# Kernel optimization log

Measured on AMD Instinct MI355X. Metric: run time of the kernel, lower is better.

## Reference

```python
import jax, jax.numpy as jnp
import numpy as np

B, S, D, L = 16, 2048, 256, 4  # batch, seq, embedding_dim, num_blocks
NUM_FEATS = 6  # time features; +1 price = 7 input channels


def _layernorm(x, g, b):
    mu = x.mean(-1, keepdims=True)
    var = x.var(-1, keepdims=True)
    return (x - mu) * jax.lax.rsqrt(var + 1e-5) * g + b


def _slstm(gx, Wh):
    """sLSTM with exponential gating + max stabilizer.
    gx: [S, B, 4D] input-side pre-activations; Wh: [D, 4D] recurrent weights.
    Returns hidden states [S, B, D]."""
    d = Wh.shape[0]
    b = gx.shape[1]
    z0 = jnp.zeros((b, d), gx.dtype)
    init = (z0, z0, z0, z0)  # c, n, h, m

    def step(carry, gx_t):
        c, n, h, m = carry
        g = gx_t + h @ Wh
        i_t, f_t, z_t, o_t = jnp.split(g, 4, axis=-1)
        m_new = jnp.maximum(f_t + m, i_t)          # stabilizer state
        i_p = jnp.exp(i_t - m_new)                 # exp input gate
        f_p = jnp.exp(f_t + m - m_new)             # exp forget gate
        c = f_p * c + i_p * jnp.tanh(z_t)
        n = f_p * n + i_p                          # normalizer
        h = jax.nn.sigmoid(o_t) * c / jnp.maximum(jnp.abs(n), 1.0)
        return (c, n, h, m_new), h

    _, hs = jax.lax.scan(step, init, gx)
    return hs


def setup_inputs() -> dict:
    key = jax.random.key(0)
    ks = jax.random.split(key, 10)
    s = 0.02
    return {
        "x": jax.random.normal(ks[0], (B, S), jnp.float32),
        "time_features": jax.random.normal(ks[1], (B, S, NUM_FEATS), jnp.float32),
        "in_W": jax.random.normal(ks[2], (NUM_FEATS + 1, D), jnp.float32) * s,
        "in_b": jnp.zeros((D,), jnp.float32),
        "ln_g": jnp.ones((L, D), jnp.float32),
        "ln_b": jnp.zeros((L, D), jnp.float32),
        "Wx": jax.random.normal(ks[3], (L, D, 4 * D), jnp.float32) * s,
        "Wh": jax.random.normal(ks[4], (L, D, 4 * D), jnp.float32) * s,
        "bg": jnp.zeros((L, 4 * D), jnp.float32),
        "fc_W": jax.random.normal(ks[5], (D, 1), jnp.float32) * s,
        "fc_b": jnp.zeros((1,), jnp.float32),
    }


def reference(x, time_features, in_W, in_b, ln_g, ln_b, Wx, Wh, bg, fc_W, fc_b):
    # concat price + time features -> [B, S, 7]; project to embedding_dim
    feats = jnp.concatenate([x[..., None], time_features], axis=-1)
    h = feats @ in_W + in_b  # [B, S, D]
    nblocks = ln_g.shape[0]
    for l in range(nblocks):  # fixed small layer count
        xn = _layernorm(h, ln_g[l], ln_b[l])
        gx = jnp.einsum("bsd,de->bse", xn, Wx[l]) + bg[l]  # [B,S,4D]
        hs = _slstm(gx.transpose(1, 0, 2), Wh[l])          # [S,B,D]
        h = h + hs.transpose(1, 0, 2)                       # residual
    # dropout is identity in eval mode
    return h[:, -1, :] @ fc_W + fc_b  # [B, 1]
```

## Files before the change

kernel.cpp:

```cpp
#include <hip/hip_runtime.h>

#define BB 16
#define SS 2048
#define DD 256
#define ND4 1024
#define PRD 16
#define PGD 8
#define HLP 4

typedef __attribute__((ext_vector_type(8))) _Float16 half8;
typedef __attribute__((ext_vector_type(4))) float f32x4;
typedef __attribute__((ext_vector_type(4))) unsigned int u32x4;
typedef unsigned long long u64;
union H8 { half8 v; unsigned int u[4]; uint4 q; };
union U4 { u32x4 v; unsigned int u[4]; };

__device__ __forceinline__ u64 aload(const u64* p) {
    return __hip_atomic_load(p, __ATOMIC_RELAXED, __HIP_MEMORY_SCOPE_AGENT);
}
__device__ __forceinline__ void astore(u64* p, u64 v) {
    __hip_atomic_store(p, v, __ATOMIC_RELAXED, __HIP_MEMORY_SCOPE_AGENT);
}
__device__ __forceinline__ void wgstore(u64* p, u64 v) {
    __hip_atomic_store(p, v, __ATOMIC_RELAXED, __HIP_MEMORY_SCOPE_WORKGROUP);
}
__device__ __forceinline__ unsigned pload(const unsigned* p) {
    return __hip_atomic_load(p, __ATOMIC_RELAXED, __HIP_MEMORY_SCOPE_AGENT);
}
__device__ __forceinline__ void pstore(unsigned* p, unsigned v) {
    __hip_atomic_store(p, v, __ATOMIC_RELAXED, __HIP_MEMORY_SCOPE_AGENT);
}
__device__ __forceinline__ int aflag(int* p) {
    return __hip_atomic_load(p, __ATOMIC_RELAXED, __HIP_MEMORY_SCOPE_AGENT);
}
__device__ __forceinline__ void sflag(int* p) {
    __hip_atomic_store(p, 1, __ATOMIC_RELAXED, __HIP_MEMORY_SCOPE_AGENT);
}
__device__ __forceinline__ unsigned short f16b(float x) {
    union { _Float16 h; unsigned short u; } c; c.h = (_Float16)x; return c.u;
}
__device__ __forceinline__ unsigned umin2(unsigned a, unsigned b) { return a < b ? a : b; }
__device__ __forceinline__ bool spinBail(int& guard, int* af) {
    if ((++guard & 63) == 0) {
        __builtin_amdgcn_s_sleep(1);
        if (guard > (1 << 18) || aflag(af)) { sflag(af); return true; }
    }
    return false;
}

__global__ void embed_kernel(const float* __restrict__ x, const float* __restrict__ tf,
                             const float* __restrict__ inW, const float* __restrict__ inb,
                             float* __restrict__ h) {
    int tok = blockIdx.x, d = threadIdx.x;
    float xv = x[tok];
    float acc = inb[d] + xv * inW[d];
#pragma unroll
    for (int c = 0; c < 6; ++c)
        acc = fmaf(tf[tok * 6 + c], inW[(c + 1) * DD + d], acc);
    h[(size_t)tok * DD + d] = acc;
}

__global__ void wxprep_kernel(const float* __restrict__ Wx, unsigned short* __restrict__ Wxh) {
    int l = blockIdx.x >> 6, G = blockIdx.x & 63;
    int lane = threadIdx.x, quad = lane >> 4, mm = lane & 15;
    const float* W = Wx + (size_t)l * DD * ND4;
    unsigned short* o = Wxh + (size_t)blockIdx.x * 4096;
#pragma unroll
    for (int kc = 0; kc < 8; ++kc) {
        __align__(16) unsigned short tmp[8];
#pragma unroll
        for (int i = 0; i < 8; ++i)
            tmp[i] = f16b(W[(size_t)(kc * 32 + quad * 8 + i) * ND4 + G * 16 + mm]);
        *(uint4*)(o + ((size_t)kc * 64 + lane) * 8) = *(uint4*)tmp;
    }
}

__global__ __launch_bounds__(256, 1) void mega_kernel(
    const float* __restrict__ hemb, const float* __restrict__ Wh,
    const float* __restrict__ lng, const float* __restrict__ lnb,
    const float* __restrict__ bgp, const unsigned short* __restrict__ Wxh,
    float* __restrict__ hout,
    u64* __restrict__ Xbuf, u64* __restrict__ Rbuf, u64* __restrict__ GXbuf,
    unsigned* __restrict__ prog, int* __restrict__ abortFlag) {
    __shared__ __align__(16) char smemBlob[57344];
    __shared__ int fastFlag;
    const int bid = blockIdx.x;
    const int tid = threadIdx.x;
    const int xslot = bid & 7;
    const int ksl = bid >> 3;
    const int l = xslot >> 1;
    const bool isScan = ((xslot & 1) == 0);
    if (!isScan && ksl >= HLP) return;

    if (isScan) {
        const int g = ksl;
        const int w = tid >> 6, lane = tid & 63;
        const int mm = lane & 15, quad = lane >> 4;
        const int sb = tid >> 4, sd = tid & 15;
        const int dglob = g * 16 + sd;
        float (*gbuf)[4][16][16] = (float (*)[4][16][16])smemBlob;

        unsigned* xt = prog + 32 + l * 16;
        if (tid == 0) {
            unsigned xcc;
            asm volatile("s_getreg_b32 %0, hwreg(HW_REG_XCC_ID)" : "=s"(xcc));
            pstore(xt + g, xcc + 1u);
        }

        H8 bfr[8];
        {
            const float* WhL = Wh + (size_t)l * DD * ND4;
            const int col = w * 256 + g * 16 + mm;
#pragma unroll
            for (int kc = 0; kc < 8; ++kc)
#pragma unroll
                for (int p = 0; p < 4; ++p) {
                    float f0 = WhL[(size_t)(32 * kc + 8 * quad + 2 * p) * ND4 + col];
                    float f1 = WhL[(size_t)(32 * kc + 8 * quad + 2 * p + 1) * ND4 + col];
                    bfr[kc].u[p] = (unsigned)f16b(f0) | ((unsigned)f16b(f1) << 16);
                }
        }

        if (tid == 0) {
            bool plOK = true;
            {
                unsigned ref = 0;
                for (int i = 0; i < 16; ++i) {
                    unsigned v = 0; int gu = 0;
                    for (;;) { v = pload(xt + i); if (v) break; if (++gu > (1 << 18)) break; }
                    if (v == 0) { plOK = false; break; }
                    if (i == 0) ref = v; else plOK &= (v == ref);
                }
            }
            unsigned* ready  = prog + 96 + l * 16;
            unsigned* result = prog + 160 + l * 16;
            u64* tw = (u64*)(prog + 24) + l;
            const u64 MAGIC = 0x5A5A5A5ADEADBEEFULL;
            if (!plOK) {
                pstore(result + g, 1u);
            } else if (g == 0) {
                int gu = 0; bool all;
                do {
                    all = true;
                    for (int i = 1; i < 16; ++i) all &= (pload(ready + i) != 0);
                } while (!all && ++gu < (1 << 20));
                wgstore(tw, MAGIC);
                pstore(result + 0, 2u);
            } else {
                u64 acc = 0;
                for (int i = 0; i < 64; ++i) acc |= *(volatile const u64*)tw;
                pstore(ready + g, 1u);
                int ok = (acc == MAGIC) ? 1 : 0, post = 0, gu = 0;
                while (!ok) {
                    u64 v;
                    asm volatile("buffer_inv sc0\n\t"
                                 "global_load_dwordx2 %0, %1, off\n\t"
                                 "s_waitcnt vmcnt(0)"
                                 : "=v"(v) : "v"(tw) : "memory");
                    if (v == MAGIC) { ok = 1; break; }
                    if (pload(result + 0) == 2u && ++post > 512) break;
                    if (++gu > (1 << 20)) break;
                }
                pstore(result + g, ok ? 2u : 1u);
            }
            bool allok = true; int gu2 = 0;
            for (int i = 0; i < 16; ++i) {
                unsigned v;
                for (;;) {
                    v = pload(result + i);
                    if (v) break;
                    if ((++gu2 & 1023) == 0) __builtin_amdgcn_s_sleep(1);
                    if (gu2 > (1 << 22)) break;
                }
                allok &= (v == 2u);
            }
            fastFlag = allok ? 1 : 0;
        }

        float c_ = 0.f, n_ = 0.f, m_ = 0.f;

        u64* Xl = Xbuf + (size_t)l * 4096;
        const u64* Rprev = Rbuf + (size_t)(l > 0 ? l - 1 : 0) * PRD * 4096;
        u64* Rcur = Rbuf + (size_t)(l < 3 ? l : 0) * PRD * 4096;
        const u64* GXl = GXbuf + (size_t)l * PGD * 16384;

        const int pquad = (dglob >> 3) & 3;
        const int ppair = (sd >> 1) & 3;
        const size_t pubIdx = (size_t)(g >> 1) * 256 + (size_t)pquad * 64 + (size_t)sb * 4 + ppair;
        const bool doPub = (sd & 1) == 0;
        const size_t rdBase = (size_t)quad * 64 + (size_t)mm * 4;
        const size_t gxIdx = (size_t)sb * 1024 + dglob;
        const size_t rIdx = (size_t)sb * 256 + dglob;
        const float* hemb0 = hemb + (size_t)sb * SS * DD + dglob;
        float* hrow = hout + (size_t)sb * SS * DD + dglob;

        unsigned psC = 0, minPgC = 0;
        const unsigned* psP = prog + (l + 1);
        const unsigned* pgP = prog + 4 + (l + 1) * 4;

        u64 pf0, pf1, pf2, pf3, pfr = 0;
        float pfh = 0.f;
        {
            const u64* Gp = GXl + gxIdx;
            pf0 = aload(Gp); pf1 = aload(Gp + 256);
            pf2 = aload(Gp + 512); pf3 = aload(Gp + 768);
            if (l > 0) pfr = aload(Rprev + rIdx);
            else pfh = hemb0[0];
        }
        __syncthreads();
        const bool fastX = (fastFlag != 0);

        auto issuePF = [&](int t1) {
            const u64* Gp1 = GXl + (size_t)(t1 & (PGD - 1)) * 16384 + gxIdx;
            pf0 = aload(Gp1); pf1 = aload(Gp1 + 256);
            pf2 = aload(Gp1 + 512); pf3 = aload(Gp1 + 768);
            if (l > 0) pfr = aload(Rprev + (size_t)(t1 & (PRD - 1)) * 4096 + rIdx);
            else pfh = hemb0[(size_t)t1 * DD];
        };

        for (int t = 0; t < SS; ++t) {
            const unsigned tagT = (unsigned)(t + 1);
            float gxi, gxf, gxz, gxoo, hin;
            {
                u64 a0 = pf0, a1 = pf1, a2 = pf2, a3 = pf3, ar = pfr;
                bool ok = ((unsigned)(a0 >> 32) == tagT) & ((unsigned)(a1 >> 32) == tagT) &
                          ((unsigned)(a2 >> 32) == tagT) & ((unsigned)(a3 >> 32) == tagT) &
                          ((l == 0) | ((unsigned)(ar >> 32) == tagT));
                if (!ok) {
                    const u64* Gp = GXl + (size_t)(t & (PGD - 1)) * 16384 + gxIdx;
                    const u64* Rp = Rprev + (size_t)(t & (PRD - 1)) * 4096 + rIdx;
                    int guard = 0;
                    for (;;) {
                        a0 = aload(Gp); a1 = aload(Gp + 256);
                        a2 = aload(Gp + 512); a3 = aload(Gp + 768);
                        if (l > 0) ar = aload(Rp);
                        ok = ((unsigned)(a0 >> 32) == tagT) & ((unsigned)(a1 >> 32) == tagT) &
                             ((unsigned)(a2 >> 32) == tagT) & ((unsigned)(a3 >> 32) == tagT) &
                             ((l == 0) | ((unsigned)(ar >> 32) == tagT));
                        if (ok) break;
                        if (spinBail(guard, abortFlag)) break;
                    }
                }
                gxi = __uint_as_float((unsigned)a0);
                gxf = __uint_as_float((unsigned)a1);
                gxz = __uint_as_float((unsigned)a2);
                gxoo = __uint_as_float((unsigned)a3);
                hin = (l > 0) ? __uint_as_float((unsigned)ar) : pfh;
            }
            f32x4 acc0 = {0.f, 0.f, 0.f, 0.f}, acc1 = {0.f, 0.f, 0.f, 0.f};
            if (t > 0) {
                const unsigned tag = (unsigned)t;
                const u64* Xp = Xl + (size_t)(t & 1) * 2048 + rdBase;
                H8 afr[8];
                if (fastX) {
                    U4 q[16];
                    const u64* b0 = Xp;
                    const u64* b1 = Xp + 512;
                    const u64* b2 = Xp + 1024;
                    const u64* b3 = Xp + 1536;
                    int guard = 0;
                    for (;;) {
                        asm volatile(
                            "buffer_inv sc0\n\t"
                            "global_load_dwordx4 %0,  %16, off\n\t"
                            "global_load_dwordx4 %1,  %16, off offset:16\n\t"
                            "global_load_dwordx4 %2,  %16, off offset:2048\n\t"
                            "global_load_dwordx4 %3,  %16, off offset:2064\n\t"
                            "global_load_dwordx4 %4,  %17, off\n\t"
                            "global_load_dwordx4 %5,  %17, off offset:16\n\t"
                            "global_load_dwordx4 %6,  %17, off offset:2048\n\t"
                            "global_load_dwordx4 %7,  %17, off offset:2064\n\t"
                            "global_load_dwordx4 %8,  %18, off\n\t"
                            "global_load_dwordx4 %9,  %18, off offset:16\n\t"
                            "global_load_dwordx4 %10, %18, off offset:2048\n\t"
                            "global_load_dwordx4 %11, %18, off offset:2064\n\t"
                            "global_load_dwordx4 %12, %19, off\n\t"
                            "global_load_dwordx4 %13, %19, off offset:16\n\t"
                            "global_load_dwordx4 %14, %19, off offset:2048\n\t"
                            "global_load_dwordx4 %15, %19, off offset:2064\n\t"
                            "s_waitcnt vmcnt(0)"
                            : "=&v"(q[0].v), "=&v"(q[1].v), "=&v"(q[2].v), "=&v"(q[3].v),
                              "=&v"(q[4].v), "=&v"(q[5].v), "=&v"(q[6].v), "=&v"(q[7].v),
                              "=&v"(q[8].v), "=&v"(q[9].v), "=&v"(q[10].v), "=&v"(q[11].v),
                              "=&v"(q[12].v), "=&v"(q[13].v), "=&v"(q[14].v), "=&v"(q[15].v)
                            : "v"(b0), "v"(b1), "v"(b2), "v"(b3)
                            : "memory");
                        bool ok = true;
#pragma unroll
                        for (int i = 0; i < 16; ++i)
                            ok &= (q[i].u[1] == tag) & (q[i].u[3] == tag);
                        if (ok) break;
                        if ((++guard & 255) == 0) {
                            if (guard > (1 << 18) || aflag(abortFlag)) { sflag(abortFlag); break; }
                        }
                    }
#pragma unroll
                    for (int kc = 0; kc < 8; ++kc) {
                        afr[kc].u[0] = q[kc * 2].u[0];
                        afr[kc].u[1] = q[kc * 2].u[2];
                        afr[kc].u[2] = q[kc * 2 + 1].u[0];
                        afr[kc].u[3] = q[kc * 2 + 1].u[2];
                    }
                } else {
                    u64 v[32];
                    int guard = 0;
                    for (;;) {
#pragma unroll
                        for (int kc = 0; kc < 8; ++kc)
#pragma unroll
                            for (int p = 0; p < 4; ++p)
                                v[kc * 4 + p] = aload(Xp + (size_t)kc * 256 + p);
                        bool ok = true;
#pragma unroll
                        for (int i = 0; i < 32; ++i) ok &= ((unsigned)(v[i] >> 32) == tag);
                        if (ok) break;
                        if ((++guard & 255) == 0) {
                            if (guard > (1 << 18) || aflag(abortFlag)) { sflag(abortFlag); break; }
                        }
                    }
#pragma unroll
                    for (int kc = 0; kc < 8; ++kc)
#pragma unroll
                        for (int p = 0; p < 4; ++p) afr[kc].u[p] = (unsigned)v[kc * 4 + p];
                }
                issuePF(t + 1 < SS ? t + 1 : t);
                acc0 = __builtin_amdgcn_mfma_f32_16x16x32_f16(afr[0].v, bfr[0].v, acc0, 0, 0, 0);
                acc1 = __builtin_amdgcn_mfma_f32_16x16x32_f16(afr[1].v, bfr[1].v, acc1, 0, 0, 0);
                acc0 = __builtin_amdgcn_mfma_f32_16x16x32_f16(afr[2].v, bfr[2].v, acc0, 0, 0, 0);
                acc1 = __builtin_amdgcn_mfma_f32_16x16x32_f16(afr[3].v, bfr[3].v, acc1, 0, 0, 0);
                acc0 = __builtin_amdgcn_mfma_f32_16x16x32_f16(afr[4].v, bfr[4].v, acc0, 0, 0, 0);
                acc1 = __builtin_amdgcn_mfma_f32_16x16x32_f16(afr[5].v, bfr[5].v, acc1, 0, 0, 0);
                acc0 = __builtin_amdgcn_mfma_f32_16x16x32_f16(afr[6].v, bfr[6].v, acc0, 0, 0, 0);
                acc1 = __builtin_amdgcn_mfma_f32_16x16x32_f16(afr[7].v, bfr[7].v, acc1, 0, 0, 0);
            } else {
                issuePF(1);
            }
            if (g == 0 && tid == 0) pstore(prog + l, (unsigned)(t + 1));
            f32x4 acc = acc0 + acc1;
            const int par = t & 1;
#pragma unroll
            for (int r = 0; r < 4; ++r) gbuf[par][w][quad * 4 + r][mm] = acc[r];
            __syncthreads();
            float gi = gbuf[par][0][sb][sd] + gxi;
            float gf = gbuf[par][1][sb][sd] + gxf;
            float gz = gbuf[par][2][sb][sd] + gxz;
            float go = gbuf[par][3][sb][sd] + gxoo;
            float mn = fmaxf(gf + m_, gi);
            float ip = __expf(gi - mn);
            float fp = __expf(gf + m_ - mn);
            float e2z = __expf(2.f * gz);
            float th = 1.f - 2.f * __builtin_amdgcn_rcpf(e2z + 1.f);
            c_ = fp * c_ + ip * th;
            n_ = fp * n_ + ip;
            m_ = mn;
            float sg = __builtin_amdgcn_rcpf(1.f + __expf(-go));
            float hval = sg * c_ * __builtin_amdgcn_rcpf(fmaxf(fabsf(n_), 1.f));
            float rnew = hin + hval;
            float hodd = __shfl_down(hval, 1);
            if (doPub) {
                unsigned payload = (unsigned)f16b(hval) | ((unsigned)f16b(hodd) << 16);
                u64 pv = ((u64)tagT << 32) | (u64)payload;
                u64* dst = Xl + (size_t)((t + 1) & 1) * 2048 + pubIdx;
                if (fastX) wgstore(dst, pv);
                else astore(dst, pv);
            }
            if (l == 3) {
                hrow[(size_t)t * DD] = rnew;
            } else {
                if (t >= PRD) {
                    unsigned needT = (unsigned)(t - PRD);
                    if (!((psC >= needT + 2) & (minPgC >= needT + 1))) {
                        int guard = 0;
                        for (;;) {
                            unsigned a  = pload(psP);
                            unsigned b0 = pload(pgP + 0);
                            unsigned b1 = pload(pgP + 1);
                            unsigned b2 = pload(pgP + 2);
                            unsigned b3 = pload(pgP + 3);
                            unsigned mn4 = umin2(umin2(b0, b1), umin2(b2, b3));
                            psC = a; minPgC = mn4;
                            if ((a >= needT + 2) & (mn4 >= needT + 1)) break;
                            if (spinBail(guard, abortFlag)) break;
                        }
                    }
                }
                astore(Rcur + (size_t)(t & (PRD - 1)) * 4096 + rIdx,
                       ((u64)tagT << 32) | (u64)__float_as_uint(rnew));
            }
            __syncthreads();
        }
    } else {
        const int j = ksl;
        const int w = tid >> 6, lane = tid & 63;
        const int mm = lane & 15, quad = lane >> 4;
        const int hb_ = tid >> 4, hd0 = (tid & 15) * 16;
        unsigned short (*hA)[264] = (unsigned short (*)[264])smemBlob;

        const u64* Rin = Rbuf + (size_t)(l > 0 ? l - 1 : 0) * PRD * 4096;
        u64* GXl = GXbuf + (size_t)l * PGD * 16384;
        const unsigned short* WxL = Wxh + (size_t)l * 262144;
        const float* lngL = lng + l * DD;
        const float* lnbL = lnb + l * DD;
        const float* bgL = bgp + (size_t)l * ND4;
        unsigned* myProg = prog + 4 + l * 4 + j;
        const unsigned* scanProg = prog + l;
        unsigned spC = 0;

        for (int t = j; t < SS; t += HLP) {
            const unsigned tagT = (unsigned)(t + 1);
            float rv[16];
            if (l == 0) {
                const float4* p = (const float4*)(hemb + ((size_t)hb_ * SS + t) * DD + hd0);
#pragma unroll
                for (int q4 = 0; q4 < 4; ++q4) {
                    float4 f = p[q4];
                    rv[q4 * 4 + 0] = f.x; rv[q4 * 4 + 1] = f.y;
                    rv[q4 * 4 + 2] = f.z; rv[q4 * 4 + 3] = f.w;
                }
            } else {
                const u64* Rp = Rin + (size_t)(t & (PRD - 1)) * 4096 + (size_t)tid * 16;
                int guard = 0;
                for (;;) {
                    u64 vv[16];
#pragma unroll
                    for (int i = 0; i < 16; ++i) vv[i] = aload(Rp + i);
                    bool ok = true;
#pragma unroll
                    for (int i = 0; i < 16; ++i) ok &= ((unsigned)(vv[i] >> 32) == tagT);
                    if (ok) {
#pragma unroll
                        for (int i = 0; i < 16; ++i) rv[i] = __uint_as_float((unsigned)vv[i]);
                        break;
                    }
                    if (spinBail(guard, abortFlag)) {
#pragma unroll
                        for (int i = 0; i < 16; ++i) rv[i] = 0.f;
                        break;
                    }
                }
            }
            float s = 0.f, ssq = 0.f;
#pragma unroll
            for (int i = 0; i < 16; ++i) { s += rv[i]; ssq += rv[i] * rv[i]; }
#pragma unroll
            for (int msk = 1; msk < 16; msk <<= 1) {
                s += __shfl_xor(s, msk);
                ssq += __shfl_xor(ssq, msk);
            }
            float muv = s * (1.f / 256.f);
            float rsv = rsqrtf(fmaxf(ssq * (1.f / 256.f) - muv * muv, 0.f) + 1e-5f);
            {
                __align__(16) unsigned short ov[16];
#pragma unroll
                for (int i = 0; i < 16; ++i)
                    ov[i] = f16b((rv[i] - muv) * rsv * lngL[hd0 + i] + lnbL[hd0 + i]);
                *(uint4*)&hA[hb_][hd0] = *(uint4*)&ov[0];
                *(uint4*)&hA[hb_][hd0 + 8] = *(uint4*)&ov[8];
            }
            __syncthreads();
            if (tid == 0) pstore(myProg, (unsigned)(t + 1));
            H8 A[8];
#pragma unroll
            for (int kc = 0; kc < 8; ++kc)
                A[kc].q = *(const uint4*)&hA[mm][kc * 32 + quad * 8];
            f32x4 acc[16];
            const unsigned short* WxW = WxL + (size_t)w * 16 * 4096;
#pragma unroll
            for (int n = 0; n < 16; ++n) {
                const unsigned short* bp = WxW + (size_t)n * 4096 + (size_t)lane * 8;
                f32x4 a = {0.f, 0.f, 0.f, 0.f};
#pragma unroll
                for (int kc = 0; kc < 8; ++kc) {
                    H8 B;
                    B.q = *(const uint4*)(bp + (size_t)kc * 512);
                    a = __builtin_amdgcn_mfma_f32_16x16x32_f16(A[kc].v, B.v, a, 0, 0, 0);
                }
                acc[n] = a;
            }
            if (t >= PGD) {
                unsigned need = (unsigned)(t - PGD) + 2;
                if (spC < need) {
                    int guard = 0;
                    for (;;) {
                        unsigned v = pload(scanProg);
                        spC = v;
                        if (v >= need) break;
                        if (spinBail(guard, abortFlag)) break;
                    }
                }
            }
            u64* Gq = GXl + (size_t)(t & (PGD - 1)) * 16384;
#pragma unroll
            for (int n = 0; n < 16; ++n) {
                int c = (w * 16 + n) * 16 + mm;
                float bgv = bgL[c];
                f32x4 a = acc[n];
#pragma unroll
                for (int r = 0; r < 4; ++r)
                    astore(Gq + (size_t)(quad * 4 + r) * 1024 + c,
                           ((u64)tagT << 32) | (u64)__float_as_uint(a[r] + bgv));
            }
            __syncthreads();
        }
    }
}

__global__ void final_kernel(const float* __restrict__ h, const float* __restrict__ fcW,
                             const float* __restrict__ fcb, float* __restrict__ out) {
    int b = blockIdx.x, lane = threadIdx.x;
    const float4 hv = *(const float4*)(h + ((size_t)b * SS + (SS - 1)) * DD + lane * 4);
    const float4 wv = *(const float4*)(fcW + lane * 4);
    float s = hv.x * wv.x + hv.y * wv.y + hv.z * wv.z + hv.w * wv.w;
#pragma unroll
    for (int off = 32; off; off >>= 1) s += __shfl_down(s, off);
    if (lane == 0) out[b] = s + fcb[0];
}

extern "C" void kernel_launch(void* const* d_in, const int* in_sizes, int n_in,
                              void* d_out, int out_size, void* d_ws, size_t ws_size,
                              hipStream_t stream) {
    const float* x   = (const float*)d_in[0];
    const float* tf  = (const float*)d_in[1];
    const float* inW = (const float*)d_in[2];
    const float* inb = (const float*)d_in[3];
    const float* lng = (const float*)d_in[4];
    const float* lnb = (const float*)d_in[5];
    const float* Wx  = (const float*)d_in[6];
    const float* Wh  = (const float*)d_in[7];
    const float* bg  = (const float*)d_in[8];
    const float* fcW = (const float*)d_in[9];
    const float* fcb = (const float*)d_in[10];
    float* out = (float*)d_out;

    const size_t nTok = (size_t)BB * SS;
    float* hemb = (float*)d_ws;
    float* hout = hemb + nTok * DD;
    unsigned short* Wxh = (unsigned short*)(hout + nTok * DD);
    u64* Xbuf = (u64*)(Wxh + 1048576);
    u64* Rbuf = Xbuf + 4 * 2 * 2048;
    u64* GXbuf = Rbuf + 3 * PRD * 4096;
    unsigned* prog = (unsigned*)(GXbuf + 4 * PGD * 16384);
    int* abortFlag = (int*)(prog + 20);

    const size_t needed = (size_t)((char*)(prog + 256) - (char*)d_ws);
    if (ws_size < needed) return;

    hipMemsetAsync(prog, 0, 256 * sizeof(unsigned), stream);

    embed_kernel<<<nTok, DD, 0, stream>>>(x, tf, inW, inb, hemb);
    wxprep_kernel<<<4 * 64, 64, 0, stream>>>(Wx, Wxh);
    mega_kernel<<<128, 256, 0, stream>>>(hemb, Wh, lng, lnb, bg, Wxh, hout,
                                         Xbuf, Rbuf, GXbuf, prog, abortFlag);
    final_kernel<<<BB, 64, 0, stream>>>(hout, fcW, fcb, out);
    (void)in_sizes; (void)n_in; (void)out_size;
}
```

Baseline: 6.804 ms.

## Replace per-element tag polling with per-block arrival counters for recurrent exchange

```diff
diff --git a/kernel.cpp b/kernel.cpp
--- a/kernel.cpp
+++ b/kernel.cpp
@@ -29,6 +29,9 @@
 }
 __device__ __forceinline__ void pstore(unsigned* p, unsigned v) {
     __hip_atomic_store(p, v, __ATOMIC_RELAXED, __HIP_MEMORY_SCOPE_AGENT);
+}
+__device__ __forceinline__ void pwgstore(unsigned* p, unsigned v) {
+    __hip_atomic_store(p, v, __ATOMIC_RELAXED, __HIP_MEMORY_SCOPE_WORKGROUP);
 }
 __device__ __forceinline__ int aflag(int* p) {
     return __hip_atomic_load(p, __ATOMIC_RELAXED, __HIP_MEMORY_SCOPE_AGENT);
@@ -134,8 +137,10 @@
             }
             unsigned* ready  = prog + 96 + l * 16;
             unsigned* result = prog + 160 + l * 16;
-            u64* tw = (u64*)(prog + 24) + l;
-            const u64 MAGIC = 0x5A5A5A5ADEADBEEFULL;
+            u64* tw = (u64*)(prog + 384 + l * 16);
+            u64* pw = (u64*)(prog + 448 + l * 16);
+            const u64 MAGIC  = 0x5A5A5A5ADEADBEEFULL;
+            const u64 MAGIC2 = 0x1234ABCD9876EF01ULL;
             if (!plOK) {
                 pstore(result + g, 1u);
             } else if (g == 0) {
@@ -144,20 +149,32 @@
                     all = true;
                     for (int i = 1; i < 16; ++i) all &= (pload(ready + i) != 0);
                 } while (!all && ++gu < (1 << 20));
+                wgstore(pw, MAGIC2);
+                asm volatile("s_waitcnt vmcnt(0)" ::: "memory");
                 wgstore(tw, MAGIC);
                 pstore(result + 0, 2u);
             } else {
-                u64 acc = 0;
+                u64 acc = 0, accp = 0;
                 for (int i = 0; i < 64; ++i) acc |= *(volatile const u64*)tw;
+                accp = *(volatile const u64*)pw;
                 pstore(ready + g, 1u);
-                int ok = (acc == MAGIC) ? 1 : 0, post = 0, gu = 0;
+                int ok = (acc == MAGIC && accp == MAGIC2) ? 1 : 0;
+                int post = 0, gu = 0;
                 while (!ok) {
                     u64 v;
                     asm volatile("buffer_inv sc0\n\t"
                                  "global_load_dwordx2 %0, %1, off\n\t"
                                  "s_waitcnt vmcnt(0)"
                                  : "=v"(v) : "v"(tw) : "memory");
-                    if (v == MAGIC) { ok = 1; break; }
+                    if (v == MAGIC) {
+                        u64 v2;
+                        asm volatile("buffer_inv sc0\n\t"
+                                     "global_load_dwordx2 %0, %1, off\n\t"
+                                     "s_waitcnt vmcnt(0)"
+                                     : "=v"(v2) : "v"(pw) : "memory");
+                        ok = (v2 == MAGIC2) ? 1 : 0;
+                        break;
+                    }
                     if (pload(result + 0) == 2u && ++post > 512) break;
                     if (++gu > (1 << 20)) break;
                 }
@@ -193,6 +210,9 @@
         const size_t rIdx = (size_t)sb * 256 + dglob;
         const float* hemb0 = hemb + (size_t)sb * SS * DD + dglob;
         float* hrow = hout + (size_t)sb * SS * DD + dglob;
+
+        const unsigned* arrL = prog + 256 + l * 16;
+        unsigned* arrW = prog + 256 + l * 16 + g;
 
         unsigned psC = 0, minPgC = 0;
         const unsigned* psP = prog + (l + 1);
@@ -253,55 +273,93 @@
                 const u64* Xp = Xl + (size_t)(t & 1) * 2048 + rdBase;
                 H8 afr[8];
                 if (fastX) {
-                    U4 q[16];
-                    const u64* b0 = Xp;
-                    const u64* b1 = Xp + 512;
-                    const u64* b2 = Xp + 1024;
-                    const u64* b3 = Xp + 1536;
-                    int guard = 0;
-                    for (;;) {
-                        asm volatile(
-                            "buffer_inv sc0\n\t"
-                            "global_load_dwordx4 %0,  %16, off\n\t"
-                            "global_load_dwordx4 %1,  %16, off offset:16\n\t"
-                            "global_load_dwordx4 %2,  %16, off offset:2048\n\t"
-                            "global_load_dwordx4 %3,  %16, off offset:2064\n\t"
-                            "global_load_dwordx4 %4,  %17, off\n\t"
-                            "global_load_dwordx4 %5,  %17, off offset:16\n\t"
-                            "global_load_dwordx4 %6,  %17, off offset:2048\n\t"
-                            "global_load_dwordx4 %7,  %17, off offset:2064\n\t"
-                            "global_load_dwordx4 %8,  %18, off\n\t"
-                            "global_load_dwordx4 %9,  %18, off offset:16\n\t"
-                            "global_load_dwordx4 %10, %18, off offset:2048\n\t"
-                            "global_load_dwordx4 %11, %18, off offset:2064\n\t"
-                            "global_load_dwordx4 %12, %19, off\n\t"
-                            "global_load_dwordx4 %13, %19, off offset:16\n\t"
-                            "global_load_dwordx4 %14, %19, off offset:2048\n\t"
-                            "global_load_dwordx4 %15, %19, off offset:2064\n\t"
-                            "s_waitcnt vmcnt(0)"
-                            : "=&v"(q[0].v), "=&v"(q[1].v), "=&v"(q[2].v), "=&v"(q[3].v),
-                              "=&v"(q[4].v), "=&v"(q[5].v), "=&v"(q[6].v), "=&v"(q[7].v),
-                              "=&v"(q[8].v), "=&v"(q[9].v), "=&v"(q[10].v), "=&v"(q[11].v),
-                              "=&v"(q[12].v), "=&v"(q[13].v), "=&v"(q[14].v), "=&v"(q[15].v)
-                            : "v"(b0), "v"(b1), "v"(b2), "v"(b3)
-                            : "memory");
-                        bool ok = true;
-#pragma unroll
-                        for (int i = 0; i < 16; ++i)
-                            ok &= (q[i].u[1] == tag) & (q[i].u[3] == tag);
-                        if (ok) break;
-                        if ((++guard & 255) == 0) {
-                            if (guard > (1 << 18) || aflag(abortFlag)) { sflag(abortFlag); break; }
+                    {
+                        const unsigned needA = (unsigned)t;
+                        int guard = 0;
+                        for (;;) {
+                            unsigned av;
+                            asm volatile("buffer_inv sc0\n\t"
+                                         "global_load_dword %0, %1, off\n\t"
+                                         "s_waitcnt vmcnt(0)"
+                                         : "=v"(av)
+                                         : "v"(arrL + (lane & 15)) : "memory");
+                            if (__all((int)(av >= needA))) break;
+                            if ((++guard & 255) == 0) {
+                                if (guard > (1 << 18) || aflag(abortFlag)) { sflag(abortFlag); break; }
+                            }
                         }
                     }
+                    bool okp = true;
 #pragma unroll
                     for (int kc = 0; kc < 8; ++kc) {
-                        afr[kc].u[0] = q[kc * 2].u[0];
-                        afr[kc].u[1] = q[kc * 2].u[2];
-                        afr[kc].u[2] = q[kc * 2 + 1].u[0];
-                        afr[kc].u[3] = q[kc * 2 + 1].u[2];
+                        const uint4* p2 = (const uint4*)(Xp + (size_t)kc * 256);
+                        uint4 qa = p2[0], qb = p2[1];
+                        afr[kc].u[0] = qa.x; afr[kc].u[1] = qa.z;
+                        afr[kc].u[2] = qb.x; afr[kc].u[3] = qb.z;
+                        okp &= (qa.y == tag) & (qa.w == tag) & (qb.y == tag) & (qb.w == tag);
+                    }
+                    if (!okp) {
+                        U4 q[16];
+                        const u64* b0 = Xp;
+                        const u64* b1 = Xp + 512;
+                        const u64* b2 = Xp + 1024;
+                        const u64* b3 = Xp + 1536;
+                        int guard = 0;
+                        for (;;) {
+                            asm volatile(
+                                "buffer_inv sc0\n\t"
+                                "global_load_dwordx4 %0,  %16, off\n\t"
+                                "global_load_dwordx4 %1,  %16, off offset:16\n\t"
+                                "global_load_dwordx4 %2,  %16, off offset:2048\n\t"
+                                "global_load_dwordx4 %3,  %16, off offset:2064\n\t"
+                                "global_load_dwordx4 %4,  %17, off\n\t"
+                                "global_load_dwordx4 %5,  %17, off offset:16\n\t"
+                                "global_load_dwordx4 %6,  %17, off offset:2048\n\t"
+                                "global_load_dwordx4 %7,  %17, off offset:2064\n\t"
+                                "global_load_dwordx4 %8,  %18, off\n\t"
+                                "global_load_dwordx4 %9,  %18, off offset:16\n\t"
+                                "global_load_dwordx4 %10, %18, off offset:2048\n\t"
+                                "global_load_dwordx4 %11, %18, off offset:2064\n\t"
+                                "global_load_dwordx4 %12, %19, off\n\t"
+                                "global_load_dwordx4 %13, %19, off offset:16\n\t"
+                                "global_load_dwordx4 %14, %19, off offset:2048\n\t"
+                                "global_load_dwordx4 %15, %19, off offset:2064\n\t"
+                                "s_waitcnt vmcnt(0)"
+                                : "=&v"(q[0].v), "=&v"(q[1].v), "=&v"(q[2].v), "=&v"(q[3].v),
+                                  "=&v"(q[4].v), "=&v"(q[5].v), "=&v"(q[6].v), "=&v"(q[7].v),
+                                  "=&v"(q[8].v), "=&v"(q[9].v), "=&v"(q[10].v), "=&v"(q[11].v),
+                                  "=&v"(q[12].v), "=&v"(q[13].v), "=&v"(q[14].v), "=&v"(q[15].v)
+                                : "v"(b0), "v"(b1), "v"(b2), "v"(b3)
+                                : "memory");
+                            bool ok = true;
+#pragma unroll
+                            for (int i = 0; i < 16; ++i)
+                                ok &= (q[i].u[1] == tag) & (q[i].u[3] == tag);
+                            if (ok) break;
+                            if ((++guard & 255) == 0) {
+                                if (guard > (1 << 18) || aflag(abortFlag)) { sflag(abortFlag); break; }
+                            }
+                        }
+#pragma unroll
+                        for (int kc = 0; kc < 8; ++kc) {
+                            afr[kc].u[0] = q[kc * 2].u[0];
+                            afr[kc].u[1] = q[kc * 2].u[2];
+                            afr[kc].u[2] = q[kc * 2 + 1].u[0];
+                            afr[kc].u[3] = q[kc * 2 + 1].u[2];
+                        }
                     }
                 } else {
+                    {
+                        const unsigned needA = (unsigned)t;
+                        int guard = 0;
+                        for (;;) {
+                            unsigned av = pload(arrL + (lane & 15));
+                            if (__all((int)(av >= needA))) break;
+                            if ((++guard & 255) == 0) {
+                                if (guard > (1 << 18) || aflag(abortFlag)) { sflag(abortFlag); break; }
+                            }
+                        }
+                    }
                     u64 v[32];
                     int guard = 0;
                     for (;;) {
@@ -364,6 +422,12 @@
                 if (fastX) wgstore(dst, pv);
                 else astore(dst, pv);
             }
+            asm volatile("s_waitcnt vmcnt(0)" ::: "memory");
+            __syncthreads();
+            if (tid == 0) {
+                if (fastX) pwgstore(arrW, tagT);
+                else pstore(arrW, tagT);
+            }
             if (l == 3) {
                 hrow[(size_t)t * DD] = rnew;
             } else {
@@ -387,7 +451,6 @@
                 astore(Rcur + (size_t)(t & (PRD - 1)) * 4096 + rIdx,
                        ((u64)tagT << 32) | (u64)__float_as_uint(rnew));
             }
-            __syncthreads();
         }
     } else {
         const int j = ksl;
@@ -542,10 +605,10 @@
     unsigned* prog = (unsigned*)(GXbuf + 4 * PGD * 16384);
     int* abortFlag = (int*)(prog + 20);
 
-    const size_t needed = (size_t)((char*)(prog + 256) - (char*)d_ws);
+    const size_t needed = (size_t)((char*)(prog + 512) - (char*)d_ws);
     if (ws_size < needed) return;
 
-    hipMemsetAsync(prog, 0, 256 * sizeof(unsigned), stream);
+    hipMemsetAsync(prog, 0, 512 * sizeof(unsigned), stream);
 
     embed_kernel<<<nTok, DD, 0, stream>>>(x, tf, inW, inb, hemb);
     wxprep_kernel<<<4 * 64, 64, 0, stream>>>(Wx, Wxh);
```

New measurement: 7.818 ms. +14.9%, slower.
